# Kernel tuning notes

Hardware: AMD Instinct MI355X
Metric: run time of the kernel (lower is better)

Reference implementation:

```python
import jax, jax.numpy as jnp
import numpy as np

N_NODES = 1048576
N_GRAPHS = 4096
NODES_PER_GRAPH = N_NODES // N_GRAPHS
N_EDGES = 8388608
F_IN = 16
HID = 32


def _glorot(k, shp):
    return jax.random.normal(k, shp, jnp.float32) * np.float32(np.sqrt(2.0 / (shp[-2] + shp[-1])))


def setup_inputs() -> dict:
    key = jax.random.key(0)
    ks = jax.random.split(key, 8)
    d = F_IN + HID  # DCRNN gate convs act on cat([X, H])
    return {
        "x": jax.random.normal(ks[0], (N_NODES, F_IN), jnp.float32),
        "edge_index": jax.random.randint(ks[1], (2, N_EDGES), 0, N_NODES),
        "edge_weight": jax.random.uniform(ks[2], (N_EDGES,), jnp.float32),
        "batch": jnp.repeat(jnp.arange(N_GRAPHS), NODES_PER_GRAPH),
        "W_z": _glorot(ks[3], (2, 1, d, HID)),
        "b_z": jnp.zeros((HID,), jnp.float32),
        "W_r": _glorot(ks[4], (2, 1, d, HID)),
        "b_r": jnp.zeros((HID,), jnp.float32),
        "W_h": _glorot(ks[5], (2, 1, d, HID)),
        "b_h": jnp.zeros((HID,), jnp.float32),
        "W_lin": _glorot(ks[6], (HID, 1)),
        "b_lin": jnp.zeros((1,), jnp.float32),
    }


def _dconv_k1(X, W, b):
    # torch_geometric_temporal DConv with K=1: the diffusion loop never runs,
    # so H = X @ W[0,0] + X @ W[1,0] + b (edge_index/edge_weight unused).
    return X @ (W[0, 0] + W[1, 0]) + b


def reference(x, edge_index, edge_weight, batch, W_z, b_z, W_r, b_r, W_h, b_h, W_lin, b_lin):
    del edge_index, edge_weight  # mathematically unused when K=1
    h0 = jnp.zeros((x.shape[0], HID), x.dtype)  # DCRNN hidden state default
    xh = jnp.concatenate([x, h0], axis=1)
    Z = jax.nn.sigmoid(_dconv_k1(xh, W_z, b_z))
    R = jax.nn.sigmoid(_dconv_k1(xh, W_r, b_r))
    xhr = jnp.concatenate([x, h0 * R], axis=1)
    H_tilde = jnp.tanh(_dconv_k1(xhr, W_h, b_h))
    H = Z * h0 + (1.0 - Z) * H_tilde  # (N, 32)
    h = jax.nn.relu(H)
    h = h @ W_lin + b_lin  # (N, 1)
    # global_mean_pool over per-node graph ids
    sums = jax.ops.segment_sum(h, batch, num_segments=N_GRAPHS)
    cnts = jax.ops.segment_sum(jnp.ones((h.shape[0], 1), h.dtype), batch, num_segments=N_GRAPHS)
    return sums / jnp.maximum(cnts, 1.0)  # (N_GRAPHS, 1)
```

## Files before the change

kernel.cpp:

```cpp
#include <hip/hip_runtime.h>

#define N_GRAPHS  4096
#define NPG       256
#define F_IN      16
#define HID       32
#define LOG2E     1.4426950408889634f

#define WS_FLOATS 1121

typedef _Float16 half8   __attribute__((ext_vector_type(8)));
typedef float    float4v __attribute__((ext_vector_type(4)));

#if __has_builtin(__builtin_amdgcn_exp2f)
#define EXP2(x) __builtin_amdgcn_exp2f(x)
#else
#define EXP2(x) exp2f(x)
#endif

union FragU { uint4 u; half8 h; };

__device__ __forceinline__ uint4 make_frag(int f, int l,
    const float* __restrict__ Wz, const float* __restrict__ Wh)
{
    const int q = l >> 4, m = l & 15;
    const int c = (f & 1) * 16 + m;
    const float s = (f < 2) ? LOG2E : 2.0f * LOG2E;
    const float* W = (f < 2) ? Wz : Wh;
    FragU u;
#pragma unroll
    for (int j = 0; j < 8; ++j) {
        const int k = (q & 1) * 8 + j;
        u.h[j] = (_Float16)((W[k * 32 + c] + W[1536 + k * 32 + c]) * s);
    }
    return u.u;
}

__global__ __launch_bounds__(256) void prep_kernel(
    const float* __restrict__ Wz, const float* __restrict__ bz,
    const float* __restrict__ Wh, const float* __restrict__ bh,
    const float* __restrict__ Wlin, const float* __restrict__ blin,
    float* __restrict__ w)
{
    const int t = threadIdx.x;
    ((uint4*)w)[t] = make_frag(t >> 6, t & 63, Wz, Wh);
    if (t < HID) {
        w[1024 + t] = bz[t] * LOG2E;
        w[1056 + t] = bh[t] * (2.0f * LOG2E);
        w[1088 + t] = Wlin[t];
    }
    if (t == 0) w[1120] = blin[0];
}

__device__ __forceinline__ float gate_term(float az, float ah, float wl, float osum)
{
    const float e1 = EXP2(az);
    const float e2 = EXP2(fminf(ah, 126.0f));
    const float r  = __builtin_amdgcn_rcpf((1.0f + e1) * (e2 + 1.0f));
    float v = (e2 - 1.0f) * r;
    v = v > 0.0f ? v : 0.0f;
    return fmaf(v, wl, osum);
}

__device__ __forceinline__ void gcn_body(const float* __restrict__ x,
                                         const float* __restrict__ w,
                                         float* __restrict__ out, int g, int t)
{
    const int lane = t & 63, wv = t >> 6;
    const int q = lane >> 4, m = lane & 15;

    const uint4* bq = (const uint4*)w;
    FragU u0, u1, u2, u3;
    u0.u = bq[lane];       u1.u = bq[64 + lane];
    u2.u = bq[128 + lane]; u3.u = bq[192 + lane];
    const half8 Bz0 = u0.h, Bz1 = u1.h, Bh0 = u2.h, Bh1 = u3.h;

    const float bz0 = w[1024 + m], bz1 = w[1040 + m];
    const float bh0 = w[1056 + m], bh1 = w[1072 + m];
    const float wl0 = w[1088 + m], wl1 = w[1104 + m];

    const float* xw = x + ((size_t)g * NPG + wv * 64 + m) * F_IN + (q & 1) * 8;
    float4 c0 = *(const float4*)(xw);
    float4 c1 = *(const float4*)(xw + 4);
    const bool lo_lane = (q >= 2);
    float osum = 0.0f;

#pragma unroll
    for (int it = 0; it < 4; ++it) {
        float4 n0 = c0, n1 = c1;
        if (it < 3) {
            n0 = *(const float4*)(xw + (it + 1) * 256);
            n1 = *(const float4*)(xw + (it + 1) * 256 + 4);
        }
        const float xf[8] = { c0.x, c0.y, c0.z, c0.w, c1.x, c1.y, c1.z, c1.w };
        half8 A;
#pragma unroll
        for (int j = 0; j < 8; ++j) {
            _Float16 h = (_Float16)xf[j];
            if (lo_lane) h = (_Float16)(xf[j] - (float)h);
            A[j] = h;
        }

        float4v az0 = { bz0, bz0, bz0, bz0 };
        float4v az1 = { bz1, bz1, bz1, bz1 };
        float4v ah0 = { bh0, bh0, bh0, bh0 };
        float4v ah1 = { bh1, bh1, bh1, bh1 };
        az0 = __builtin_amdgcn_mfma_f32_16x16x32_f16(A, Bz0, az0, 0, 0, 0);
        ah0 = __builtin_amdgcn_mfma_f32_16x16x32_f16(A, Bh0, ah0, 0, 0, 0);
        az1 = __builtin_amdgcn_mfma_f32_16x16x32_f16(A, Bz1, az1, 0, 0, 0);
        ah1 = __builtin_amdgcn_mfma_f32_16x16x32_f16(A, Bh1, ah1, 0, 0, 0);

#pragma unroll
        for (int i = 0; i < 4; ++i) {
            osum = gate_term(az0[i], ah0[i], wl0, osum);
            osum = gate_term(az1[i], ah1[i], wl1, osum);
        }
        c0 = n0; c1 = n1;
    }

#pragma unroll
    for (int off = 32; off > 0; off >>= 1)
        osum += __shfl_down(osum, off, 64);
    __shared__ float part[4];
    if (lane == 0) part[wv] = osum;
    __syncthreads();
    if (t == 0)
        out[g] = (part[0] + part[1] + part[2] + part[3]) * (1.0f / (float)NPG)
               + w[1120];
}

__global__ __launch_bounds__(256, 6) void gcn_main(
    const float* __restrict__ x, const float* __restrict__ w, float* __restrict__ out)
{
    gcn_body(x, w, out, blockIdx.x, threadIdx.x);
}

__global__ __launch_bounds__(256, 6) void gcn_main_lds(
    const float* __restrict__ x,
    const float* __restrict__ Wz, const float* __restrict__ bz,
    const float* __restrict__ Wh, const float* __restrict__ bh,
    const float* __restrict__ Wlin, const float* __restrict__ blin,
    float* __restrict__ out)
{
    __shared__ __attribute__((aligned(16))) float w[WS_FLOATS];
    const int t = threadIdx.x;
    ((uint4*)w)[t] = make_frag(t >> 6, t & 63, Wz, Wh);
    if (t < HID) {
        w[1024 + t] = bz[t] * LOG2E;
        w[1056 + t] = bh[t] * (2.0f * LOG2E);
        w[1088 + t] = Wlin[t];
    }
    if (t == 0) w[1120] = blin[0];
    __syncthreads();
    gcn_body(x, w, out, blockIdx.x, t);
}

extern "C" void kernel_launch(void* const* d_in, const int* in_sizes, int n_in,
                              void* d_out, int out_size, void* d_ws, size_t ws_size,
                              hipStream_t stream)
{
    const float* x    = (const float*)d_in[0];
    const float* Wz   = (const float*)d_in[4];
    const float* bz   = (const float*)d_in[5];
    const float* Wh   = (const float*)d_in[8];
    const float* bh   = (const float*)d_in[9];
    const float* Wlin = (const float*)d_in[10];
    const float* blin = (const float*)d_in[11];
    float* out = (float*)d_out;

    if (ws_size >= WS_FLOATS * sizeof(float)) {
        float* w = (float*)d_ws;
        prep_kernel<<<1, 256, 0, stream>>>(Wz, bz, Wh, bh, Wlin, blin, w);
        gcn_main<<<N_GRAPHS, NPG, 0, stream>>>(x, w, out);
    } else {
        gcn_main_lds<<<N_GRAPHS, NPG, 0, stream>>>(x, Wz, bz, Wh, bh, Wlin, blin, out);
    }
}
```

Measured before the change: 166.6 us.

## Switch gate GEMM to 32x32x16 MFMA with split-fp16 hi/lo passes

Replaces the 16x16x32 MFMA tiling, which packed the fp16 hi and lo parts of x into the K dimension, with 32x32x16 MFMAs. Each tile now runs separate hi and lo passes covering all 32 hidden columns, so each wave handles two 32-node tiles instead of four 16-node iterations. The packed weight fragments shrink to two per lane and all x loads are issued up front. The change reduces the MFMA instruction count and the fragment registers, but the 16-wide accumulators raise register pressure, so the occupancy hint drops from 6 to 5.

```diff
diff --git a/kernel.cpp b/kernel.cpp
--- a/kernel.cpp
+++ b/kernel.cpp
@@ -6,10 +6,10 @@
 #define HID       32
 #define LOG2E     1.4426950408889634f
 
-#define WS_FLOATS 1121
+#define WS_FLOATS 609
 
-typedef _Float16 half8   __attribute__((ext_vector_type(8)));
-typedef float    float4v __attribute__((ext_vector_type(4)));
+typedef _Float16 half8  __attribute__((ext_vector_type(8)));
+typedef float    f32x16 __attribute__((ext_vector_type(16)));
 
 #if __has_builtin(__builtin_amdgcn_exp2f)
 #define EXP2(x) __builtin_amdgcn_exp2f(x)
@@ -19,18 +19,17 @@
 
 union FragU { uint4 u; half8 h; };
 
-__device__ __forceinline__ uint4 make_frag(int f, int l,
+__device__ __forceinline__ uint4 make_frag32(int f, int l,
     const float* __restrict__ Wz, const float* __restrict__ Wh)
 {
-    const int q = l >> 4, m = l & 15;
-    const int c = (f & 1) * 16 + m;
-    const float s = (f < 2) ? LOG2E : 2.0f * LOG2E;
-    const float* W = (f < 2) ? Wz : Wh;
+    const int col = l & 31, p = l >> 5;
+    const float s = (f == 0) ? LOG2E : 2.0f * LOG2E;
+    const float* W = (f == 0) ? Wz : Wh;
     FragU u;
 #pragma unroll
     for (int j = 0; j < 8; ++j) {
-        const int k = (q & 1) * 8 + j;
-        u.h[j] = (_Float16)((W[k * 32 + c] + W[1536 + k * 32 + c]) * s);
+        const int k = p * 8 + j;
+        u.h[j] = (_Float16)((W[k * 32 + col] + W[1536 + k * 32 + col]) * s);
     }
     return u.u;
 }
@@ -42,13 +41,13 @@
     float* __restrict__ w)
 {
     const int t = threadIdx.x;
-    ((uint4*)w)[t] = make_frag(t >> 6, t & 63, Wz, Wh);
+    if (t < 128) ((uint4*)w)[t] = make_frag32(t >> 6, t & 63, Wz, Wh);
     if (t < HID) {
-        w[1024 + t] = bz[t] * LOG2E;
-        w[1056 + t] = bh[t] * (2.0f * LOG2E);
-        w[1088 + t] = Wlin[t];
+        w[512 + t] = bz[t] * LOG2E;
+        w[544 + t] = bh[t] * (2.0f * LOG2E);
+        w[576 + t] = Wlin[t];
     }
-    if (t == 0) w[1120] = blin[0];
+    if (t == 0) w[608] = blin[0];
 }
 
 __device__ __forceinline__ float gate_term(float az, float ah, float wl, float osum)
@@ -61,61 +60,54 @@
     return fmaf(v, wl, osum);
 }
 
+__device__ __forceinline__ float tile32(float4 c0, float4 c1,
+    half8 Bz, half8 Bh, float bzl, float bhl, float wll, float osum)
+{
+    const float xf[8] = { c0.x, c0.y, c0.z, c0.w, c1.x, c1.y, c1.z, c1.w };
+    half8 Ah, Al;
+#pragma unroll
+    for (int j = 0; j < 8; ++j) {
+        const _Float16 h = (_Float16)xf[j];
+        Ah[j] = h;
+        Al[j] = (_Float16)(xf[j] - (float)h);
+    }
+    f32x16 accZ, accH;
+#pragma unroll
+    for (int i = 0; i < 16; ++i) { accZ[i] = bzl; accH[i] = bhl; }
+    accZ = __builtin_amdgcn_mfma_f32_32x32x16_f16(Ah, Bz, accZ, 0, 0, 0);
+    accH = __builtin_amdgcn_mfma_f32_32x32x16_f16(Ah, Bh, accH, 0, 0, 0);
+    accZ = __builtin_amdgcn_mfma_f32_32x32x16_f16(Al, Bz, accZ, 0, 0, 0);
+    accH = __builtin_amdgcn_mfma_f32_32x32x16_f16(Al, Bh, accH, 0, 0, 0);
+#pragma unroll
+    for (int i = 0; i < 16; ++i)
+        osum = gate_term(accZ[i], accH[i], wll, osum);
+    return osum;
+}
+
 __device__ __forceinline__ void gcn_body(const float* __restrict__ x,
                                          const float* __restrict__ w,
                                          float* __restrict__ out, int g, int t)
 {
     const int lane = t & 63, wv = t >> 6;
-    const int q = lane >> 4, m = lane & 15;
+    const int col = lane & 31, p = lane >> 5;
 
     const uint4* bq = (const uint4*)w;
-    FragU u0, u1, u2, u3;
-    u0.u = bq[lane];       u1.u = bq[64 + lane];
-    u2.u = bq[128 + lane]; u3.u = bq[192 + lane];
-    const half8 Bz0 = u0.h, Bz1 = u1.h, Bh0 = u2.h, Bh1 = u3.h;
+    FragU uz, uh;
+    uz.u = bq[lane];
+    uh.u = bq[64 + lane];
 
-    const float bz0 = w[1024 + m], bz1 = w[1040 + m];
-    const float bh0 = w[1056 + m], bh1 = w[1072 + m];
-    const float wl0 = w[1088 + m], wl1 = w[1104 + m];
+    const float bzl = w[512 + col];
+    const float bhl = w[544 + col];
+    const float wll = w[576 + col];
 
-    const float* xw = x + ((size_t)g * NPG + wv * 64 + m) * F_IN + (q & 1) * 8;
-    float4 c0 = *(const float4*)(xw);
-    float4 c1 = *(const float4*)(xw + 4);
-    const bool lo_lane = (q >= 2);
-    float osum = 0.0f;
+    const float* xw = x + ((size_t)g * NPG + wv * 64 + col) * F_IN + p * 8;
+    const float4 a0 = *(const float4*)(xw);
+    const float4 a1 = *(const float4*)(xw + 4);
+    const float4 b0 = *(const float4*)(xw + 512);
+    const float4 b1 = *(const float4*)(xw + 512 + 4);
 
-#pragma unroll
-    for (int it = 0; it < 4; ++it) {
-        float4 n0 = c0, n1 = c1;
-        if (it < 3) {
-            n0 = *(const float4*)(xw + (it + 1) * 256);
-            n1 = *(const float4*)(xw + (it + 1) * 256 + 4);
-        }
-        const float xf[8] = { c0.x, c0.y, c0.z, c0.w, c1.x, c1.y, c1.z, c1.w };
-        half8 A;
-#pragma unroll
-        for (int j = 0; j < 8; ++j) {
-            _Float16 h = (_Float16)xf[j];
-            if (lo_lane) h = (_Float16)(xf[j] - (float)h);
-            A[j] = h;
-        }
-
-        float4v az0 = { bz0, bz0, bz0, bz0 };
-        float4v az1 = { bz1, bz1, bz1, bz1 };
-        float4v ah0 = { bh0, bh0, bh0, bh0 };
-        float4v ah1 = { bh1, bh1, bh1, bh1 };
-        az0 = __builtin_amdgcn_mfma_f32_16x16x32_f16(A, Bz0, az0, 0, 0, 0);
-        ah0 = __builtin_amdgcn_mfma_f32_16x16x32_f16(A, Bh0, ah0, 0, 0, 0);
-        az1 = __builtin_amdgcn_mfma_f32_16x16x32_f16(A, Bz1, az1, 0, 0, 0);
-        ah1 = __builtin_amdgcn_mfma_f32_16x16x32_f16(A, Bh1, ah1, 0, 0, 0);
-
-#pragma unroll
-        for (int i = 0; i < 4; ++i) {
-            osum = gate_term(az0[i], ah0[i], wl0, osum);
-            osum = gate_term(az1[i], ah1[i], wl1, osum);
-        }
-        c0 = n0; c1 = n1;
-    }
+    float osum = tile32(a0, a1, uz.h, uh.h, bzl, bhl, wll, 0.0f);
+    osum       = tile32(b0, b1, uz.h, uh.h, bzl, bhl, wll, osum);
 
 #pragma unroll
     for (int off = 32; off > 0; off >>= 1)
@@ -125,16 +117,16 @@
     __syncthreads();
     if (t == 0)
         out[g] = (part[0] + part[1] + part[2] + part[3]) * (1.0f / (float)NPG)
-               + w[1120];
+               + w[608];
 }
 
-__global__ __launch_bounds__(256, 6) void gcn_main(
+__global__ __launch_bounds__(256, 5) void gcn_main(
     const float* __restrict__ x, const float* __restrict__ w, float* __restrict__ out)
 {
     gcn_body(x, w, out, blockIdx.x, threadIdx.x);
 }
 
-__global__ __launch_bounds__(256, 6) void gcn_main_lds(
+__global__ __launch_bounds__(256, 5) void gcn_main_lds(
     const float* __restrict__ x,
     const float* __restrict__ Wz, const float* __restrict__ bz,
     const float* __restrict__ Wh, const float* __restrict__ bh,
@@ -143,13 +135,13 @@
 {
     __shared__ __attribute__((aligned(16))) float w[WS_FLOATS];
     const int t = threadIdx.x;
-    ((uint4*)w)[t] = make_frag(t >> 6, t & 63, Wz, Wh);
+    if (t < 128) ((uint4*)w)[t] = make_frag32(t >> 6, t & 63, Wz, Wh);
     if (t < HID) {
-        w[1024 + t] = bz[t] * LOG2E;
-        w[1056 + t] = bh[t] * (2.0f * LOG2E);
-        w[1088 + t] = Wlin[t];
+        w[512 + t] = bz[t] * LOG2E;
+        w[544 + t] = bh[t] * (2.0f * LOG2E);
+        w[576 + t] = Wlin[t];
     }
-    if (t == 0) w[1120] = blin[0];
+    if (t == 0) w[608] = blin[0];
     __syncthreads();
     gcn_body(x, w, out, blockIdx.x, t);
 }
```

New measurement: 178.4 us. 1.07x slower.
